# Optimization experiments

Measured on AMD Instinct MI355X. Metric: run time of the kernel, lower is better.

## Reference

```python
import jax, jax.numpy as jnp
import numpy as np

# MORRConfig_20um_MQ (all-pass MRR) constants used by mrr_roundtrip_phase_to_tr(intensity=True)
A = 0.987   # attenuation_factor a
R = 0.99    # coupling_factor r
KS, STRIDE, PAD = 3, 1, 1
IN_C, OUT_C, MB = 32, 64, 8


def _unfold(x, ks, pad, stride):
    # torch.nn.functional.unfold: output channel order is (C, kh, kw), C slowest
    B, C, H, W = x.shape
    xp = jnp.pad(x, ((0, 0), (0, 0), (pad, pad), (pad, pad)))
    Ho = (H + 2 * pad - ks) // stride + 1
    Wo = (W + 2 * pad - ks) // stride + 1
    cols = jnp.stack(
        [xp[:, :, i:i + stride * Ho:stride, j:j + stride * Wo:stride]
         for i in range(ks) for j in range(ks)],
        axis=2,
    )  # [B, C, ks*ks, Ho, Wo]
    return cols.reshape(B, C * ks * ks, Ho * Wo), Ho, Wo


def _mrr_tr(phase):
    # all-pass MRR intensity transmission vs roundtrip phase detuning
    c = jnp.cos(phase)
    return (A * A - 2.0 * A * R * c + R * R) / (1.0 - 2.0 * A * R * c + (A * R) ** 2)


def setup_inputs() -> dict:
    key = jax.random.key(0)
    k1, k2, k3 = jax.random.split(key, 3)
    B, H, W = 8, 64, 64
    wic = IN_C * KS * KS           # 288, divisible by miniblock -> no zero pad
    q = wic // MB                  # grid_dim_x = 36
    p = OUT_C // MB                # grid_dim_y = 8
    x = jax.random.normal(k1, (B, IN_C, H, W), jnp.float32)
    weight = jax.random.normal(k2, (p, q, MB), jnp.float32)
    morr_output_scale = jax.random.normal(k3, (max(1, q // 2) + 1,), jnp.float32)
    return {"x": x, "weight": weight, "morr_output_scale": morr_output_scale}


def reference(x, weight, morr_output_scale):
    B = x.shape[0]
    p, q, k = weight.shape
    w = jnp.abs(weight)                                  # w_bit=16 -> build_weight() = |W|
    cols, Ho, Wo = _unfold(x, KS, PAD, STRIDE)           # [B, wic, L]
    xf = cols.transpose(0, 2, 1).reshape(-1, q, k)       # [N, q, k], N = B*Ho*Wo
    xf = xf * xf                                         # intensity modulation x^2
    # block-circulant matvec via rFFT (circular convolution per (p, q) block)
    Xf = jnp.fft.rfft(xf, n=k, axis=-1)                  # [N, q, kf]
    Wf = jnp.fft.rfft(w, n=k, axis=-1)                   # [p, q, kf]
    phase = jnp.fft.irfft(Xf[:, None, :, :] * Wf[None, :, :, :], n=k, axis=-1)  # [N, p, q, k]
    tr = _mrr_tr(phase)                                  # MORR nonlinear transfer
    # differential-rail output scale (even grid_dim_x branch)
    s = morr_output_scale
    if q % 2 == 0:
        scale = jnp.concatenate([s[:-1], -s[:-1]])
    else:
        scale = jnp.concatenate([s[:-1], s[-1:], -s[:-1]])
    out = jnp.einsum('npqk,q->npk', tr, scale).reshape(-1, p * k)[:, :OUT_C]
    return out.reshape(B, Ho, Wo, OUT_C).transpose(0, 3, 1, 2)  # [B, OUT_C, Ho, Wo]
```

## Files before the change

kernel.cpp:

```cpp
#include <hip/hip_runtime.h>
#include <math.h>
#include <utility>


template <class F, size_t... I>
__device__ __forceinline__ void sf_impl(F&& f, std::index_sequence<I...>) {
    (f(std::integral_constant<size_t, I>{}), ...);
}
template <size_t N, class F>
__device__ __forceinline__ void static_for(F&& f) {
    sf_impl(f, std::make_index_sequence<N>{});
}

__global__ __launch_bounds__(1024, 8)
void morr_kernel(const float* __restrict__ xg, const float* __restrict__ wg,
                 const float* __restrict__ sg, float* __restrict__ out) {
    __shared__ __align__(16) float smx[32 * 10 * 40];

    constexpr double Ad = 0.987, Rd = 0.99;
    constexpr float K2  = (float)(2.0 * Ad * Rd);
    constexpr float C2  = (float)(1.0 + (Ad * Rd) * (Ad * Rd));
    constexpr float NDK = (float)(-(1.0 - Ad * Ad) * (1.0 - Rd * Rd) * (2.0 * Ad * Rd));
    constexpr float INV2PI = 0.15915494309189535f;

    const int tid = threadIdx.x;
    const int b   = blockIdx.z;
    const int gr0 = blockIdx.y * 8;
    const int gc0 = blockIdx.x * 8;

    for (int i = tid; i < 3200; i += 1024) {
        int c = i / 100, rem = i - c * 100;
        int r = rem / 10, cl = rem - r * 10;
        int gr = gr0 - 1 + r, gc = gc0 - 1 + cl;
        float v = 0.f;
        if ((unsigned)gr < 64u && (unsigned)gc < 64u)
            v = xg[((b * 32 + c) * 64 + gr) * 64 + gc];
        smx[c * 400 + r * 40 + cl] = v * v * INV2PI;
    }
    __syncthreads();

    const int px  = tid & 63;
    const int th4 = __builtin_amdgcn_readfirstlane(((tid >> 6) & 1) * 4);
    const int p   = __builtin_amdgcn_readfirstlane(tid >> 7);
    const int row = px >> 3;
    const int col = px & 7;

    const float* __restrict__ xb = &smx[row * 40 + col];
    const unsigned* __restrict__ wgu =
        reinterpret_cast<const unsigned*>(wg) + p * 288;

    float acc[4];
    static_for<4>([&](auto J) { acc[J] = 0.f; });

    static_for<18>([&](auto QP) {
        constexpr int qp = QP;
        float xl[8], xh[8];
        static_for<8>([&](auto S) {
            constexpr int s   = S;
            constexpr int u   = qp * 8 + s;
            constexpr int off = (u / 9) * 400 + ((u % 9) / 3) * 40 + (u % 3);
            xl[s] = xb[off];
            xh[s] = xb[off + 6400];
        });
        float wl[8], wh[8];
        static_for<8>([&](auto Jw) {
            constexpr int j = Jw;
            wl[j] = __uint_as_float(wgu[qp * 8 + (j ^ th4)] & 0x7fffffffu);
            wh[j] = __uint_as_float(wgu[144 + qp * 8 + (j ^ th4)] & 0x7fffffffu);
        });
        const float sv = sg[qp];

        static_for<4>([&](auto J) {
            constexpr int t = J;
            float p1 = xl[0] * wl[t];
            float p2 = xh[0] * wh[t];
            static_for<7>([&](auto S) {
                constexpr int s = (int)S + 1;
                p1 = fmaf(xl[s], wl[(t - s + 8) & 7], p1);
                p2 = fmaf(xh[s], wh[(t - s + 8) & 7], p2);
            });
            float c1 = __builtin_amdgcn_cosf(p1);
            float c2 = __builtin_amdgcn_cosf(p2);
            float a  = fmaf(-K2, c1, C2);
            float bb = fmaf(-K2, c2, C2);
            float rr = __builtin_amdgcn_rcpf(a * bb);
            acc[J] = fmaf(sv, (c1 - c2) * rr, acc[J]);
        });
    });

    const int gr = gr0 + row, gc = gc0 + col;
    static_for<4>([&](auto J) {
        constexpr int j = J;
        const int oc = p * 8 + th4 + j;
        out[((b * 64 + oc) * 64 + gr) * 64 + gc] = NDK * acc[j];
    });
}

extern "C" void kernel_launch(void* const* d_in, const int* in_sizes, int n_in,
                              void* d_out, int out_size, void* d_ws, size_t ws_size,
                              hipStream_t stream) {
    const float* x = (const float*)d_in[0];
    const float* w = (const float*)d_in[1];
    const float* s = (const float*)d_in[2];
    float* out = (float*)d_out;
    dim3 grid(8, 8, 8);
    dim3 block(1024);
    hipLaunchKernelGGL(morr_kernel, grid, block, 0, stream, x, w, s, out);
}
```

Before: 92.18 us.

## Compute circulant phase products with split-fp16 MFMA and a pre-expanded weight table

The per-thread scalar FMA circular convolution is replaced by 16x16x32 fp16 MFMA instructions. Inputs and weights are split into high and low fp16 halves, and three MFMAs per tile recover near-fp32 accuracy. A separate prep kernel expands the circulant weight matrix into a workspace table, and output is staged through shared memory for coalesced stores. This targets the FMA cost of the phase computation, but adds a second launch, possible precision error in the cosine argument, and a smaller 256-thread block.

Result: slower. 103.1 us (+11.8%).

```diff
diff --git a/kernel.cpp b/kernel.cpp
--- a/kernel.cpp
+++ b/kernel.cpp
@@ -1,7 +1,13 @@
 #include <hip/hip_runtime.h>
+#include <hip/hip_fp16.h>
 #include <math.h>
 #include <utility>
 
+
+typedef _Float16 f16x8 __attribute__((ext_vector_type(8)));
+typedef float    f32x4 __attribute__((ext_vector_type(4)));
+typedef unsigned int u32;
+typedef u32 u32x4 __attribute__((ext_vector_type(4)));
 
 template <class F, size_t... I>
 __device__ __forceinline__ void sf_impl(F&& f, std::index_sequence<I...>) {
@@ -12,88 +18,151 @@
     sf_impl(f, std::make_index_sequence<N>{});
 }
 
-__global__ __launch_bounds__(1024, 8)
-void morr_kernel(const float* __restrict__ xg, const float* __restrict__ wg,
-                 const float* __restrict__ sg, float* __restrict__ out) {
-    __shared__ __align__(16) float smx[32 * 10 * 40];
+__device__ __forceinline__ u32 pck(float a, float b) {
+    _Float16 ha = (_Float16)a, hb = (_Float16)b;
+    return (u32)__builtin_bit_cast(unsigned short, ha) |
+           ((u32)__builtin_bit_cast(unsigned short, hb) << 16);
+}
+
+#define INV2PI 0.15915494309189535f
+
+__global__ void bprep(const float* __restrict__ wg, u32* __restrict__ bt) {
+    int tid = blockIdx.x * 256 + threadIdx.x;
+    int nthr = gridDim.x * 256;
+    for (int e = tid; e < 288 * 68; e += nthr) {
+        int slot = e / 68, wi = e - slot * 68;
+        u32 val = 0u;
+        if (wi < 64) {
+            int hl = slot & 1, qpt = slot >> 1;
+            int q = qpt >> 2, pt = qpt & 3;
+            int l = wi >> 2, jp = wi & 3;
+            int flat = pt * 16 + l, p = flat >> 3, t = flat & 7;
+            float wa = fabsf(wg[(p * 36 + q) * 8 + ((t - 2 * jp) & 7)]) * INV2PI;
+            float wb = fabsf(wg[(p * 36 + q) * 8 + ((t - 2 * jp - 1) & 7)]) * INV2PI;
+            _Float16 ha = (_Float16)wa, hb = (_Float16)wb;
+            if (hl == 0) {
+                val = pck((float)ha, (float)hb);
+            } else {
+                val = pck(wa - (float)ha, wb - (float)hb);
+            }
+        }
+        bt[e] = val;
+    }
+}
+
+__global__ __launch_bounds__(256, 4)
+void morr_mfma(const float* __restrict__ xg, const u32* __restrict__ bt,
+               const float* __restrict__ sg, float* __restrict__ out) {
+    __shared__ union {
+        u32   x[3200];
+        float o[64 * 65];
+    } sm;
 
     constexpr double Ad = 0.987, Rd = 0.99;
     constexpr float K2  = (float)(2.0 * Ad * Rd);
     constexpr float C2  = (float)(1.0 + (Ad * Rd) * (Ad * Rd));
     constexpr float NDK = (float)(-(1.0 - Ad * Ad) * (1.0 - Rd * Rd) * (2.0 * Ad * Rd));
-    constexpr float INV2PI = 0.15915494309189535f;
 
     const int tid = threadIdx.x;
     const int b   = blockIdx.z;
-    const int gr0 = blockIdx.y * 8;
-    const int gc0 = blockIdx.x * 8;
+    const int gr0 = blockIdx.y * 8, gc0 = blockIdx.x * 8;
 
-    for (int i = tid; i < 3200; i += 1024) {
+    for (int i = tid; i < 3200; i += 256) {
         int c = i / 100, rem = i - c * 100;
         int r = rem / 10, cl = rem - r * 10;
         int gr = gr0 - 1 + r, gc = gc0 - 1 + cl;
         float v = 0.f;
         if ((unsigned)gr < 64u && (unsigned)gc < 64u)
             v = xg[((b * 32 + c) * 64 + gr) * 64 + gc];
-        smx[c * 400 + r * 40 + cl] = v * v * INV2PI;
+        v = v * v;
+        _Float16 h = (_Float16)v;
+        sm.x[i] = pck((float)h, v - (float)h);
     }
     __syncthreads();
 
-    const int px  = tid & 63;
-    const int th4 = __builtin_amdgcn_readfirstlane(((tid >> 6) & 1) * 4);
-    const int p   = __builtin_amdgcn_readfirstlane(tid >> 7);
-    const int row = px >> 3;
-    const int col = px & 7;
+    const int lane = tid & 63;
+    const int wv   = tid >> 6;
+    const int c16  = lane & 15;
+    const int pix  = wv * 16 + c16;
+    const int abase = (pix >> 3) * 10 + (pix & 7);
+    const int lnw  = (lane < 16) ? (lane << 2) : 64;
 
-    const float* __restrict__ xb = &smx[row * 40 + col];
-    const unsigned* __restrict__ wgu =
-        reinterpret_cast<const unsigned*>(wg) + p * 288;
+    float oacc[4][4];
+    static_for<4>([&](auto P) { static_for<4>([&](auto R) { oacc[P][R] = 0.f; }); });
 
-    float acc[4];
-    static_for<4>([&](auto J) { acc[J] = 0.f; });
+    #pragma unroll 1
+    for (int qp = 0; qp < 18; ++qp) {
+        const int q0 = qp, q1 = qp + 18;
+        u32 xw0[8], xw1[8];
+        static_for<8>([&](auto J) {
+            constexpr int j = J;
+            const int ci0 = q0 * 8 + j, c0 = ci0 / 9, rm0 = ci0 - c0 * 9;
+            const int ci1 = q1 * 8 + j, c1 = ci1 / 9, rm1 = ci1 - c1 * 9;
+            xw0[j] = sm.x[abase + c0 * 100 + (rm0 / 3) * 10 + (rm0 - (rm0 / 3) * 3)];
+            xw1[j] = sm.x[abase + c1 * 100 + (rm1 / 3) * 10 + (rm1 - (rm1 / 3) * 3)];
+        });
+        u32x4 a0h, a0l, a1h, a1l;
+        static_for<4>([&](auto JP) {
+            constexpr int jp = JP;
+            a0h[jp] = (xw0[2 * jp] & 0xFFFFu) | (xw0[2 * jp + 1] << 16);
+            a0l[jp] = (xw0[2 * jp] >> 16) | (xw0[2 * jp + 1] & 0xFFFF0000u);
+            a1h[jp] = (xw1[2 * jp] & 0xFFFFu) | (xw1[2 * jp + 1] << 16);
+            a1l[jp] = (xw1[2 * jp] >> 16) | (xw1[2 * jp + 1] & 0xFFFF0000u);
+        });
+        const f16x8 A0h = __builtin_bit_cast(f16x8, a0h);
+        const f16x8 A0l = __builtin_bit_cast(f16x8, a0l);
+        const f16x8 A1h = __builtin_bit_cast(f16x8, a1h);
+        const f16x8 A1l = __builtin_bit_cast(f16x8, a1l);
 
-    static_for<18>([&](auto QP) {
-        constexpr int qp = QP;
-        float xl[8], xh[8];
-        static_for<8>([&](auto S) {
-            constexpr int s   = S;
-            constexpr int u   = qp * 8 + s;
-            constexpr int off = (u / 9) * 400 + ((u % 9) / 3) * 40 + (u % 3);
-            xl[s] = xb[off];
-            xh[s] = xb[off + 6400];
+        f32x4 ph0[4], ph1[4];
+        static_for<4>([&](auto PT) {
+            constexpr int pt = PT;
+            const u32x4 b0h = *reinterpret_cast<const u32x4*>(bt + ((q0 * 4 + pt) * 2 + 0) * 68 + lnw);
+            const u32x4 b0l = *reinterpret_cast<const u32x4*>(bt + ((q0 * 4 + pt) * 2 + 1) * 68 + lnw);
+            const u32x4 b1h = *reinterpret_cast<const u32x4*>(bt + ((q1 * 4 + pt) * 2 + 0) * 68 + lnw);
+            const u32x4 b1l = *reinterpret_cast<const u32x4*>(bt + ((q1 * 4 + pt) * 2 + 1) * 68 + lnw);
+            f32x4 z = {0.f, 0.f, 0.f, 0.f};
+            f32x4 acc0 = __builtin_amdgcn_mfma_f32_16x16x32_f16(A0l, __builtin_bit_cast(f16x8, b0h), z, 0, 0, 0);
+            acc0 = __builtin_amdgcn_mfma_f32_16x16x32_f16(A0h, __builtin_bit_cast(f16x8, b0l), acc0, 0, 0, 0);
+            acc0 = __builtin_amdgcn_mfma_f32_16x16x32_f16(A0h, __builtin_bit_cast(f16x8, b0h), acc0, 0, 0, 0);
+            f32x4 acc1 = __builtin_amdgcn_mfma_f32_16x16x32_f16(A1l, __builtin_bit_cast(f16x8, b1h), z, 0, 0, 0);
+            acc1 = __builtin_amdgcn_mfma_f32_16x16x32_f16(A1h, __builtin_bit_cast(f16x8, b1l), acc1, 0, 0, 0);
+            acc1 = __builtin_amdgcn_mfma_f32_16x16x32_f16(A1h, __builtin_bit_cast(f16x8, b1h), acc1, 0, 0, 0);
+            ph0[pt] = acc0;
+            ph1[pt] = acc1;
         });
-        float wl[8], wh[8];
-        static_for<8>([&](auto Jw) {
-            constexpr int j = Jw;
-            wl[j] = __uint_as_float(wgu[qp * 8 + (j ^ th4)] & 0x7fffffffu);
-            wh[j] = __uint_as_float(wgu[144 + qp * 8 + (j ^ th4)] & 0x7fffffffu);
+
+        const float sv = sg[qp];
+        static_for<4>([&](auto PT) {
+            constexpr int pt = PT;
+            static_for<4>([&](auto R) {
+                constexpr int r = R;
+                float cA = __builtin_amdgcn_cosf(ph0[pt][r]);
+                float cB = __builtin_amdgcn_cosf(ph1[pt][r]);
+                float da = fmaf(-K2, cA, C2);
+                float db = fmaf(-K2, cB, C2);
+                float rr = __builtin_amdgcn_rcpf(da * db);
+                oacc[pt][r] = fmaf(sv, (cA - cB) * rr, oacc[pt][r]);
+            });
         });
-        const float sv = sg[qp];
+    }
 
-        static_for<4>([&](auto J) {
-            constexpr int t = J;
-            float p1 = xl[0] * wl[t];
-            float p2 = xh[0] * wh[t];
-            static_for<7>([&](auto S) {
-                constexpr int s = (int)S + 1;
-                p1 = fmaf(xl[s], wl[(t - s + 8) & 7], p1);
-                p2 = fmaf(xh[s], wh[(t - s + 8) & 7], p2);
-            });
-            float c1 = __builtin_amdgcn_cosf(p1);
-            float c2 = __builtin_amdgcn_cosf(p2);
-            float a  = fmaf(-K2, c1, C2);
-            float bb = fmaf(-K2, c2, C2);
-            float rr = __builtin_amdgcn_rcpf(a * bb);
-            acc[J] = fmaf(sv, (c1 - c2) * rr, acc[J]);
+    __syncthreads();
+    static_for<4>([&](auto PT) {
+        constexpr int pt = PT;
+        static_for<4>([&](auto R) {
+            constexpr int r = R;
+            const int oc  = pt * 16 + c16;
+            const int pxr = wv * 16 + (lane >> 4) * 4 + r;
+            sm.o[oc * 65 + pxr] = NDK * oacc[pt][r];
         });
     });
-
-    const int gr = gr0 + row, gc = gc0 + col;
-    static_for<4>([&](auto J) {
-        constexpr int j = J;
-        const int oc = p * 8 + th4 + j;
-        out[((b * 64 + oc) * 64 + gr) * 64 + gc] = NDK * acc[j];
-    });
+    __syncthreads();
+    for (int i = 0; i < 16; ++i) {
+        int flat = i * 256 + tid;
+        int oc = flat >> 6, px = flat & 63;
+        out[((b * 64 + oc) * 64 + gr0 + (px >> 3)) * 64 + gc0 + (px & 7)] = sm.o[oc * 65 + px];
+    }
 }
 
 extern "C" void kernel_launch(void* const* d_in, const int* in_sizes, int n_in,
@@ -102,8 +171,9 @@
     const float* x = (const float*)d_in[0];
     const float* w = (const float*)d_in[1];
     const float* s = (const float*)d_in[2];
-    float* out = (float*)d_out;
+    float* outp = (float*)d_out;
+    u32* bt = (u32*)d_ws;
+    hipLaunchKernelGGL(bprep, dim3(32), dim3(256), 0, stream, w, bt);
     dim3 grid(8, 8, 8);
-    dim3 block(1024);
-    hipLaunchKernelGGL(morr_kernel, grid, block, 0, stream, x, w, s, out);
+    hipLaunchKernelGGL(morr_mfma, grid, dim3(256), 0, stream, x, bt, s, outp);
 }
```
